# Performance work log

Measured on AMD Instinct MI355X. Metric: run time of the kernel, lower is better.

The kernel has to match this reference:

```python
import jax, jax.numpy as jnp
import numpy as np

N_NODES = 200000   # input_geom points
N_QUERY = 131072   # latent query points
K_NBR   = 32       # neighbors per query (uniform CSR for reproducibility)
N_EDGE  = N_QUERY * K_NBR
DIM     = 3
FEAT    = 3 + 2 * DIM  # N_i, D_avg, D_var, Delta(3), PCA eigvals(3)
HID     = 64
OUT     = 128


def setup_inputs() -> dict:
    key = jax.random.key(0)
    ks = jax.random.split(key, 8)
    input_geom = jax.random.normal(ks[0], (N_NODES, DIM), jnp.float32)
    latent_queries = jax.random.normal(ks[1], (N_QUERY, DIM), jnp.float32)
    neighbors_index = jax.random.randint(ks[2], (N_EDGE,), 0, N_NODES, dtype=jnp.int32)
    # uniform CSR row splits: every query has exactly K_NBR neighbors
    neighbors_row_splits = jnp.arange(N_QUERY + 1, dtype=jnp.int32) * K_NBR
    W1 = jax.random.normal(ks[3], (FEAT, HID), jnp.float32) / np.sqrt(FEAT)
    b1 = jax.random.normal(ks[4], (HID,), jnp.float32) * 0.01
    W2 = jax.random.normal(ks[5], (HID, OUT), jnp.float32) / np.sqrt(HID)
    b2 = jax.random.normal(ks[6], (OUT,), jnp.float32) * 0.01
    return {"input_geom": input_geom, "latent_queries": latent_queries,
            "neighbors_index": neighbors_index, "neighbors_row_splits": neighbors_row_splits,
            "W1": W1, "b1": b1, "W2": W2, "b2": b2}


def _stat_features(input_geom, latent_queries, neighbors_index, neighbors_row_splits):
    Q = latent_queries.shape[0]
    counts = neighbors_row_splits[1:] - neighbors_row_splits[:-1]          # [Q]
    qidx = jnp.repeat(jnp.arange(Q), counts, total_repeat_length=neighbors_index.shape[0])  # [E]
    nbr = input_geom[neighbors_index]                                      # [E, D]
    diff = nbr - latent_queries[qidx]                                      # [E, D]
    dist = jnp.linalg.norm(diff, axis=1)                                   # [E]

    N_i = counts.astype(jnp.float32)                                       # [Q]
    denom = jnp.maximum(N_i, 1.0)
    seg = lambda v: jax.ops.segment_sum(v, qidx, num_segments=Q)

    D_avg = seg(dist) / denom                                              # E[X]
    E_X2 = seg(dist * dist) / denom                                        # E[X^2]
    D_var = jnp.maximum(E_X2 - D_avg * D_avg, 0.0)

    centroid = seg(nbr) / denom[:, None]                                   # [Q, D]
    Delta = centroid - latent_queries                                      # [Q, D]

    centered = nbr - centroid[qidx]                                        # [E, D]
    cov = seg(centered[:, :, None] * centered[:, None, :]) / denom[:, None, None]  # [Q, D, D]

    eig = jnp.linalg.eigvalsh(cov)[:, ::-1]                                # descending, [Q, D]
    has = N_i > 0
    PCA = jnp.where(has[:, None], eig, 0.0)

    feat = jnp.concatenate([N_i[:, None], D_avg[:, None], D_var[:, None], Delta, PCA], axis=1)  # [Q, 9]
    feat = jnp.where(has[:, None], feat, 0.0)

    mean = feat.mean(axis=0, keepdims=True)
    std = feat.std(axis=0, ddof=1, keepdims=True)                          # torch.std is unbiased
    std = jnp.where(std < 1e-6, 1.0, std)
    return (feat - mean) / std


def reference(input_geom, latent_queries, neighbors_index, neighbors_row_splits, W1, b1, W2, b2):
    feat = _stat_features(input_geom, latent_queries, neighbors_index, neighbors_row_splits)
    h = jax.nn.relu(feat @ W1 + b1)
    return jax.nn.relu(h @ W2 + b2)
```

## Files before the change

### kernel.cpp

```cpp
#include <hip/hip_runtime.h>
#include <math.h>

#define QN 131072
#define NF 9
#define NH 64
#define NO 128
#define QT 128

using v8s = __attribute__((ext_vector_type(8))) short;
using v4f = __attribute__((ext_vector_type(4))) float;

__device__ __forceinline__ unsigned short f2bf(float x) {
  unsigned u = __float_as_uint(x);
  unsigned r = u + 0x7fffu + ((u >> 16) & 1u);
  return (unsigned short)(r >> 16);
}

__global__ __launch_bounds__(256)
void prep_kernel(const float* __restrict__ geom, float4* __restrict__ g4, int nn,
                 int padBlocks,
                 const float* __restrict__ W2, unsigned short* __restrict__ w2f,
                 float* __restrict__ acc)
{
  const int t = threadIdx.x;
  const int b = blockIdx.x;
  if (b == 0 && t < 2*NF) acc[t] = 0.0f;
  if (b < padBlocks) {
    int i = b * 256 + t;
    if (i < nn) {
      const float* p = geom + (size_t)i * 3;
      g4[i] = make_float4(p[0], p[1], p[2], 0.f);
    }
  } else {
    int i = (b - padBlocks) * 256 + t;
    int j  = i & 7;
    int l  = (i >> 3) & 63;
    int ot = (i >> 9) & 7;
    int kt = (i >> 12) & 1;
    int row = kt*32 + (l >> 4)*8 + j;
    int col = ot*16 + (l & 15);
    w2f[i] = f2bf(W2[row*NO + col]);
  }
}

__global__ __launch_bounds__(256)
void stats_kernel(const float4* __restrict__ g4,
                  const float* __restrict__ lq,
                  const int* __restrict__ nidx,
                  const int* __restrict__ rsplit,
                  float* __restrict__ feat,
                  float* __restrict__ acc)
{
  const int t = threadIdx.x;
  const int j = t & 1;
  const int q = blockIdx.x * 128 + (t >> 1);

  const int s = rsplit[q];
  const int cnt = rsplit[q+1] - s;

  const int* ip = nidx + s + j*16;
  int4 a0 = *(const int4*)(ip     );
  int4 a1 = *(const int4*)(ip +  4);
  int4 a2 = *(const int4*)(ip +  8);
  int4 a3 = *(const int4*)(ip + 12);

  const float qx = lq[q*3+0], qy = lq[q*3+1], qz = lq[q*3+2];

  int ids[16] = {a0.x,a0.y,a0.z,a0.w, a1.x,a1.y,a1.z,a1.w,
                 a2.x,a2.y,a2.z,a2.w, a3.x,a3.y,a3.z,a3.w};
  float4 P[16];
#pragma unroll
  for (int m = 0; m < 16; ++m) P[m] = g4[ids[m]];

  float sx=0.f, sy=0.f, sz=0.f;
  float sxx=0.f, sxy=0.f, sxz=0.f, syy=0.f, syz=0.f, szz=0.f;
  float sd=0.f, sd2=0.f;
#pragma unroll
  for (int m = 0; m < 16; ++m) {
    float4 p = P[m];
    sx += p.x; sy += p.y; sz += p.z;
    sxx = fmaf(p.x,p.x,sxx); sxy = fmaf(p.x,p.y,sxy); sxz = fmaf(p.x,p.z,sxz);
    syy = fmaf(p.y,p.y,syy); syz = fmaf(p.y,p.z,syz); szz = fmaf(p.z,p.z,szz);
    float dx = p.x-qx, dy = p.y-qy, dz = p.z-qz;
    float dd = fmaf(dx,dx,fmaf(dy,dy,dz*dz));
    sd2 += dd;
    sd += sqrtf(dd);
  }

  sx  += __shfl_xor(sx,  1);
  sy  += __shfl_xor(sy,  1);
  sz  += __shfl_xor(sz,  1);
  sxx += __shfl_xor(sxx, 1);
  sxy += __shfl_xor(sxy, 1);
  sxz += __shfl_xor(sxz, 1);
  syy += __shfl_xor(syy, 1);
  syz += __shfl_xor(syz, 1);
  szz += __shfl_xor(szz, 1);
  sd  += __shfl_xor(sd,  1);
  sd2 += __shfl_xor(sd2, 1);

  float cntf = (float)cnt;
  float denom = fmaxf(cntf, 1.0f);
  float inv = 1.0f / denom;
  float Davg = sd * inv;
  float Dvar = fmaxf(sd2 * inv - Davg*Davg, 0.0f);
  float cx = sx*inv, cy = sy*inv, cz = sz*inv;

  float a00 = sxx*inv - cx*cx;
  float a01 = sxy*inv - cx*cy;
  float a02 = sxz*inv - cx*cz;
  float a11 = syy*inv - cy*cy;
  float a12 = syz*inv - cy*cz;
  float a22 = szz*inv - cz*cz;

  float l0, l1, l2;
  {
    float p1 = a01*a01 + a02*a02 + a12*a12;
    float qm = (a00 + a11 + a22) * (1.0f/3.0f);
    float b00 = a00 - qm, b11 = a11 - qm, b22 = a22 - qm;
    float p2 = b00*b00 + b11*b11 + b22*b22 + 2.0f*p1;
    if (p2 < 1e-12f) {
      l0 = l1 = l2 = qm;
    } else {
      float p = sqrtf(p2 * (1.0f/6.0f));
      float ip2 = 1.0f / p;
      float c00 = b00*ip2, c11 = b11*ip2, c22 = b22*ip2;
      float c01 = a01*ip2, c02 = a02*ip2, c12 = a12*ip2;
      float det = c00*(c11*c22 - c12*c12)
                - c01*(c01*c22 - c12*c02)
                + c02*(c01*c12 - c11*c02);
      float r = fminf(1.0f, fmaxf(-1.0f, 0.5f*det));
      float phi = acosf(r) * (1.0f/3.0f);
      float tp = 2.0f * p;
      l0 = qm + tp * __cosf(phi);
      l2 = qm + tp * __cosf(phi + 2.0943951023931953f);
      l1 = 3.0f*qm - l0 - l2;
    }
  }

  float ft[NF];
  if (cntf > 0.f) {
    ft[0] = cntf; ft[1] = Davg; ft[2] = Dvar;
    ft[3] = cx - qx; ft[4] = cy - qy; ft[5] = cz - qz;
    ft[6] = l0; ft[7] = l1; ft[8] = l2;
  } else {
#pragma unroll
    for (int f = 0; f < NF; ++f) ft[f] = 0.f;
  }

  if (j == 0) {
    float* fp = feat + (size_t)q * 12;
    *(float4*)(fp    ) = make_float4(ft[0], ft[1], ft[2], ft[3]);
    *(float4*)(fp + 4) = make_float4(ft[4], ft[5], ft[6], ft[7]);
    *(float4*)(fp + 8) = make_float4(ft[8], 0.f, 0.f, 0.f);
  }

  __shared__ float sacc[4][2*NF];
  const int wid = t >> 6, lane = t & 63;
#pragma unroll
  for (int f = 0; f < NF; ++f) {
    float s1 = ft[f];
    float s2 = ft[f]*ft[f];
#pragma unroll
    for (int msk = 2; msk < 64; msk <<= 1) {
      s1 += __shfl_xor(s1, msk);
      s2 += __shfl_xor(s2, msk);
    }
    if (lane == 0) { sacc[wid][f] = s1; sacc[wid][NF+f] = s2; }
  }
  __syncthreads();
  if (t < 2*NF) {
    float ssum = sacc[0][t] + sacc[1][t] + sacc[2][t] + sacc[3][t];
    atomicAdd(&acc[t], ssum);
  }
}

__global__ __launch_bounds__(256)
void mlp_kernel(const float* __restrict__ feat,
                const float* __restrict__ acc,
                const float* __restrict__ W1, const float* __restrict__ b1,
                const unsigned short* __restrict__ w2f,
                const float* __restrict__ b2,
                float* __restrict__ out)
{
  __shared__ float sW1[NF*NH];
  __shared__ float sb1[NH];
  __shared__ float sb2[NO];
  __shared__ float ssc[NF], sbi[NF];
  __shared__ __align__(16) unsigned short ldsA[8*2*64*8];
  __shared__ __align__(16) unsigned short ldsB[2*8*64*8];

  const int t = threadIdx.x;
  const int qbase = blockIdx.x * QT;

  for (int i = t; i < NF*NH; i += 256) sW1[i] = W1[i];
  if (t < NH) sb1[t] = b1[t];
  if (t >= 64 && t < 64+NO) sb2[t-64] = b2[t-64];
  for (int i = t; i < 4096; i += 256) ((uint*)ldsB)[i] = ((const uint*)w2f)[i];
  if (t >= 192 && t < 192+NF) {
    int f = t - 192;
    double s = (double)acc[f], s2 = (double)acc[NF+f];
    const double Qd = (double)QN;
    double mean = s / Qd;
    double var = fmax((s2 - s*s/Qd) / (Qd - 1.0), 0.0);
    double sd = sqrt(var);
    if (sd < 1e-6) sd = 1.0;
    double iscl = 1.0 / sd;
    ssc[f] = (float)iscl;
    sbi[f] = (float)(-mean * iscl);
  }
  __syncthreads();

#pragma unroll
  for (int pass = 0; pass < 4; ++pass) {
    int item = pass*256 + t;
    int q  = item & 127;
    int kc = item >> 7;
    const float* fp = feat + (size_t)(qbase + q) * 12;
    float4 f0 = *(const float4*)(fp);
    float4 f1 = *(const float4*)(fp + 4);
    float f8v = fp[8];
    float fv[NF];
    fv[0] = fmaf(f0.x, ssc[0], sbi[0]);
    fv[1] = fmaf(f0.y, ssc[1], sbi[1]);
    fv[2] = fmaf(f0.z, ssc[2], sbi[2]);
    fv[3] = fmaf(f0.w, ssc[3], sbi[3]);
    fv[4] = fmaf(f1.x, ssc[4], sbi[4]);
    fv[5] = fmaf(f1.y, ssc[5], sbi[5]);
    fv[6] = fmaf(f1.z, ssc[6], sbi[6]);
    fv[7] = fmaf(f1.w, ssc[7], sbi[7]);
    fv[8] = fmaf(f8v,  ssc[8], sbi[8]);

    float h[8];
#pragma unroll
    for (int jj = 0; jj < 8; ++jj) h[jj] = sb1[kc*8 + jj];
#pragma unroll
    for (int k = 0; k < NF; ++k) {
      float fk = fv[k];
#pragma unroll
      for (int jj = 0; jj < 8; ++jj)
        h[jj] = fmaf(fk, sW1[k*NH + kc*8 + jj], h[jj]);
    }
    uint pk[4];
#pragma unroll
    for (int jj = 0; jj < 4; ++jj) {
      unsigned short lo = f2bf(fmaxf(h[2*jj  ], 0.f));
      unsigned short hi = f2bf(fmaxf(h[2*jj+1], 0.f));
      pk[jj] = (uint)lo | ((uint)hi << 16);
    }
    int base = ((((q >> 4)*2 + (kc >> 2))*64) + (q & 15) + 16*(kc & 3)) * 8;
    *(uint4*)&ldsA[base] = make_uint4(pk[0], pk[1], pk[2], pk[3]);
  }
  __syncthreads();

  const int wave = t >> 6;
  const int lane = t & 63;
  const int col  = lane & 15;
  const int rb   = (lane >> 4) * 4;

  v8s B00 = *(v8s*)&ldsB[(((0*8) + 2*wave    )*64 + lane)*8];
  v8s B01 = *(v8s*)&ldsB[(((0*8) + 2*wave + 1)*64 + lane)*8];
  v8s B10 = *(v8s*)&ldsB[(((1*8) + 2*wave    )*64 + lane)*8];
  v8s B11 = *(v8s*)&ldsB[(((1*8) + 2*wave + 1)*64 + lane)*8];

  const int o0 = (2*wave    )*16 + col;
  const int o1 = (2*wave + 1)*16 + col;
  const float b2a = sb2[o0];
  const float b2b = sb2[o1];

#pragma unroll
  for (int qt = 0; qt < 8; ++qt) {
    v8s A0 = *(v8s*)&ldsA[((qt*2 + 0)*64 + lane)*8];
    v8s A1 = *(v8s*)&ldsA[((qt*2 + 1)*64 + lane)*8];
    v4f c0 = {0.f, 0.f, 0.f, 0.f};
    v4f c1 = {0.f, 0.f, 0.f, 0.f};
    c0 = __builtin_amdgcn_mfma_f32_16x16x32_bf16(A0, B00, c0, 0, 0, 0);
    c0 = __builtin_amdgcn_mfma_f32_16x16x32_bf16(A1, B10, c0, 0, 0, 0);
    c1 = __builtin_amdgcn_mfma_f32_16x16x32_bf16(A0, B01, c1, 0, 0, 0);
    c1 = __builtin_amdgcn_mfma_f32_16x16x32_bf16(A1, B11, c1, 0, 0, 0);
#pragma unroll
    for (int r = 0; r < 4; ++r) {
      int gq = qbase + qt*16 + rb + r;
      out[(size_t)gq*NO + o0] = fmaxf(c0[r] + b2a, 0.f);
      out[(size_t)gq*NO + o1] = fmaxf(c1[r] + b2b, 0.f);
    }
  }
}

extern "C" void kernel_launch(void* const* d_in, const int* in_sizes, int n_in,
                              void* d_out, int out_size, void* d_ws, size_t ws_size,
                              hipStream_t stream) {
  const float* geom = (const float*)d_in[0];
  const float* lq   = (const float*)d_in[1];
  const int*   nidx = (const int*)d_in[2];
  const int*   rspl = (const int*)d_in[3];
  const float* W1   = (const float*)d_in[4];
  const float* b1   = (const float*)d_in[5];
  const float* W2   = (const float*)d_in[6];
  const float* b2   = (const float*)d_in[7];
  float* out = (float*)d_out;
  const int nn = in_sizes[0] / 3;

  char* w = (char*)d_ws;
  float*  feat = (float*)w;            w += (size_t)QN*12*sizeof(float);
  float4* g4   = (float4*)w;           w += (size_t)nn*sizeof(float4);
  unsigned short* w2f = (unsigned short*)w;  w += 16384*sizeof(unsigned short);
  float* acc   = (float*)w;

  const int padBlocks = (nn + 255) / 256;
  prep_kernel<<<padBlocks + 64, 256, 0, stream>>>(geom, g4, nn, padBlocks, W2, w2f, acc);
  stats_kernel<<<QN/128, 256, 0, stream>>>(g4, lq, nidx, rspl, feat, acc);
  mlp_kernel<<<QN/QT, 256, 0, stream>>>(feat, acc, W1, b1, w2f, b2, out);
}
```

Baseline: 133.2 us.

## Fuse prep, stats and MLP into one cooperative persistent kernel with grid syncs

Replaces the three kernel launches with one cooperative kernel of 512 blocks. It uses grid-wide syncs between the geometry padding, the statistics pass and the normalization-plus-MLP phase. Each block keeps its 256 queries' features in LDS instead of writing them to global memory and reading them back, which removes the feat round trip and two launch gaps. The gather is also split into two batches of 8 to reduce register pressure. The cost is two grid barriers, less parallelism from only 512 blocks, and a fallback to the old path if the cooperative launch fails.

```diff
diff --git a/kernel.cpp b/kernel.cpp
--- a/kernel.cpp
+++ b/kernel.cpp
@@ -1,11 +1,14 @@
 #include <hip/hip_runtime.h>
+#include <hip/hip_cooperative_groups.h>
 #include <math.h>
+
+namespace cg = cooperative_groups;
 
 #define QN 131072
 #define NF 9
 #define NH 64
 #define NO 128
-#define QT 128
+#define NBLK 512
 
 using v8s = __attribute__((ext_vector_type(8))) short;
 using v4f = __attribute__((ext_vector_type(4))) float;
@@ -14,6 +17,291 @@
   unsigned u = __float_as_uint(x);
   unsigned r = u + 0x7fffu + ((u >> 16) & 1u);
   return (unsigned short)(r >> 16);
+}
+
+__device__ __forceinline__ void eig3(float a00, float a01, float a02,
+                                     float a11, float a12, float a22,
+                                     float& l0, float& l1, float& l2) {
+  float p1 = a01*a01 + a02*a02 + a12*a12;
+  float qm = (a00 + a11 + a22) * (1.0f/3.0f);
+  float b00 = a00 - qm, b11 = a11 - qm, b22 = a22 - qm;
+  float p2 = b00*b00 + b11*b11 + b22*b22 + 2.0f*p1;
+  if (p2 < 1e-12f) {
+    l0 = l1 = l2 = qm;
+  } else {
+    float p = sqrtf(p2 * (1.0f/6.0f));
+    float ip2 = 1.0f / p;
+    float c00 = b00*ip2, c11 = b11*ip2, c22 = b22*ip2;
+    float c01 = a01*ip2, c02 = a02*ip2, c12 = a12*ip2;
+    float det = c00*(c11*c22 - c12*c12)
+              - c01*(c01*c22 - c12*c02)
+              + c02*(c01*c12 - c11*c02);
+    float r = fminf(1.0f, fmaxf(-1.0f, 0.5f*det));
+    float phi = acosf(r) * (1.0f/3.0f);
+    float tp = 2.0f * p;
+    l0 = qm + tp * __cosf(phi);
+    l2 = qm + tp * __cosf(phi + 2.0943951023931953f);
+    l1 = 3.0f*qm - l0 - l2;
+  }
+}
+
+__device__ __forceinline__ void stat_query(const float4* __restrict__ g4,
+                                           const float* __restrict__ lq,
+                                           const int* __restrict__ nidx,
+                                           const int* __restrict__ rsplit,
+                                           int q, int j, float* ft) {
+  const int s = rsplit[q];
+  const int cnt = rsplit[q+1] - s;
+
+  const int* ip = nidx + s + j*16;
+  int4 a0 = *(const int4*)(ip     );
+  int4 a1 = *(const int4*)(ip +  4);
+  int4 a2 = *(const int4*)(ip +  8);
+  int4 a3 = *(const int4*)(ip + 12);
+
+  const float qx = lq[q*3+0], qy = lq[q*3+1], qz = lq[q*3+2];
+
+  float sx=0.f, sy=0.f, sz=0.f;
+  float sxx=0.f, sxy=0.f, sxz=0.f, syy=0.f, syz=0.f, szz=0.f;
+  float sd=0.f, sd2=0.f;
+
+  int idsA[8] = {a0.x,a0.y,a0.z,a0.w, a1.x,a1.y,a1.z,a1.w};
+  int idsB[8] = {a2.x,a2.y,a2.z,a2.w, a3.x,a3.y,a3.z,a3.w};
+  float4 P[8];
+#pragma unroll
+  for (int m = 0; m < 8; ++m) P[m] = g4[idsA[m]];
+#pragma unroll
+  for (int m = 0; m < 8; ++m) {
+    float4 p = P[m];
+    sx += p.x; sy += p.y; sz += p.z;
+    sxx = fmaf(p.x,p.x,sxx); sxy = fmaf(p.x,p.y,sxy); sxz = fmaf(p.x,p.z,sxz);
+    syy = fmaf(p.y,p.y,syy); syz = fmaf(p.y,p.z,syz); szz = fmaf(p.z,p.z,szz);
+    float dx = p.x-qx, dy = p.y-qy, dz = p.z-qz;
+    float dd = fmaf(dx,dx,fmaf(dy,dy,dz*dz));
+    sd2 += dd; sd += sqrtf(dd);
+  }
+#pragma unroll
+  for (int m = 0; m < 8; ++m) P[m] = g4[idsB[m]];
+#pragma unroll
+  for (int m = 0; m < 8; ++m) {
+    float4 p = P[m];
+    sx += p.x; sy += p.y; sz += p.z;
+    sxx = fmaf(p.x,p.x,sxx); sxy = fmaf(p.x,p.y,sxy); sxz = fmaf(p.x,p.z,sxz);
+    syy = fmaf(p.y,p.y,syy); syz = fmaf(p.y,p.z,syz); szz = fmaf(p.z,p.z,szz);
+    float dx = p.x-qx, dy = p.y-qy, dz = p.z-qz;
+    float dd = fmaf(dx,dx,fmaf(dy,dy,dz*dz));
+    sd2 += dd; sd += sqrtf(dd);
+  }
+
+  sx  += __shfl_xor(sx,  1);
+  sy  += __shfl_xor(sy,  1);
+  sz  += __shfl_xor(sz,  1);
+  sxx += __shfl_xor(sxx, 1);
+  sxy += __shfl_xor(sxy, 1);
+  sxz += __shfl_xor(sxz, 1);
+  syy += __shfl_xor(syy, 1);
+  syz += __shfl_xor(syz, 1);
+  szz += __shfl_xor(szz, 1);
+  sd  += __shfl_xor(sd,  1);
+  sd2 += __shfl_xor(sd2, 1);
+
+  float cntf = (float)cnt;
+  float denom = fmaxf(cntf, 1.0f);
+  float inv = 1.0f / denom;
+  float Davg = sd * inv;
+  float Dvar = fmaxf(sd2 * inv - Davg*Davg, 0.0f);
+  float cx = sx*inv, cy = sy*inv, cz = sz*inv;
+
+  float l0, l1, l2;
+  eig3(sxx*inv - cx*cx, sxy*inv - cx*cy, sxz*inv - cx*cz,
+       syy*inv - cy*cy, syz*inv - cy*cz, szz*inv - cz*cz, l0, l1, l2);
+
+  if (cntf > 0.f) {
+    ft[0] = cntf; ft[1] = Davg; ft[2] = Dvar;
+    ft[3] = cx - qx; ft[4] = cy - qy; ft[5] = cz - qz;
+    ft[6] = l0; ft[7] = l1; ft[8] = l2;
+  } else {
+#pragma unroll
+    for (int f = 0; f < NF; ++f) ft[f] = 0.f;
+  }
+}
+
+__global__ __launch_bounds__(256, 2)
+void fused_kernel(const float* __restrict__ geom,
+                  const float* __restrict__ lq,
+                  const int* __restrict__ nidx,
+                  const int* __restrict__ rsplit,
+                  const float* __restrict__ W1,
+                  const float* __restrict__ b1,
+                  const float* __restrict__ W2,
+                  const float* __restrict__ b2,
+                  float4* __restrict__ g4,
+                  unsigned short* __restrict__ w2f,
+                  float* __restrict__ acc,
+                  float* __restrict__ out,
+                  int nn)
+{
+  __shared__ __align__(16) unsigned short ldsA[8*2*64*8];
+  __shared__ float sfeat[256][NF];
+  __shared__ float sW1[NF*NH];
+  __shared__ float sb1[NH];
+  __shared__ float sb2[NO];
+  __shared__ float sacc[4][2*NF];
+  __shared__ float ssc[NF], sbi[NF];
+
+  cg::grid_group grid = cg::this_grid();
+  const int t = threadIdx.x;
+  const int b = blockIdx.x;
+  const int wave = t >> 6;
+  const int lane = t & 63;
+
+  for (int gt = b*256 + t; gt < nn; gt += NBLK*256) {
+    const float* p = geom + (size_t)gt * 3;
+    g4[gt] = make_float4(p[0], p[1], p[2], 0.f);
+  }
+  if (b == 0) {
+    if (t < 2*NF) acc[t] = 0.f;
+#pragma unroll
+    for (int grp = 0; grp < 8; ++grp) {
+      int gi = grp*256 + t;
+      int l  = gi & 63;
+      int ot = (gi >> 6) & 7;
+      int kt = (gi >> 9) & 1;
+      int col  = ot*16 + (l & 15);
+      int rowb = kt*32 + (l >> 4)*8;
+      uint pk[4];
+#pragma unroll
+      for (int jj = 0; jj < 4; ++jj) {
+        uint lo = f2bf(W2[(rowb + 2*jj    )*NO + col]);
+        uint hi = f2bf(W2[(rowb + 2*jj + 1)*NO + col]);
+        pk[jj] = lo | (hi << 16);
+      }
+      *(uint4*)&w2f[(size_t)gi*8] = make_uint4(pk[0], pk[1], pk[2], pk[3]);
+    }
+  }
+  for (int i = t; i < NF*NH; i += 256) sW1[i] = W1[i];
+  if (t < NH) sb1[t] = b1[t];
+  if (t >= 64 && t < 64+NO) sb2[t-64] = b2[t-64];
+
+  grid.sync();
+
+#pragma unroll
+  for (int tt = 0; tt < 2; ++tt) {
+    const int j  = t & 1;
+    const int ql = t >> 1;
+    const int q  = b*256 + tt*128 + ql;
+
+    float ft[NF];
+    stat_query(g4, lq, nidx, rsplit, q, j, ft);
+
+    if (j == 0) {
+#pragma unroll
+      for (int f = 0; f < NF; ++f) sfeat[tt*128 + ql][f] = ft[f];
+    }
+
+#pragma unroll
+    for (int f = 0; f < NF; ++f) {
+      float s1 = ft[f];
+      float s2 = ft[f]*ft[f];
+#pragma unroll
+      for (int msk = 2; msk < 64; msk <<= 1) {
+        s1 += __shfl_xor(s1, msk);
+        s2 += __shfl_xor(s2, msk);
+      }
+      if (lane == 0) { sacc[wave][f] = s1; sacc[wave][NF+f] = s2; }
+    }
+    __syncthreads();
+    if (t < 2*NF) {
+      float ssum = sacc[0][t] + sacc[1][t] + sacc[2][t] + sacc[3][t];
+      atomicAdd(&acc[t], ssum);
+    }
+    __syncthreads();
+  }
+
+  grid.sync();
+
+  if (t >= 192 && t < 192+NF) {
+    int f = t - 192;
+    double s = (double)acc[f], s2 = (double)acc[NF+f];
+    const double Qd = (double)QN;
+    double mean = s / Qd;
+    double var = fmax((s2 - s*s/Qd) / (Qd - 1.0), 0.0);
+    double sdv = sqrt(var);
+    if (sdv < 1e-6) sdv = 1.0;
+    double iscl = 1.0 / sdv;
+    ssc[f] = (float)iscl;
+    sbi[f] = (float)(-mean * iscl);
+  }
+  __syncthreads();
+
+  v8s B00 = ((const v8s*)w2f)[(0*8 + 2*wave    )*64 + lane];
+  v8s B01 = ((const v8s*)w2f)[(0*8 + 2*wave + 1)*64 + lane];
+  v8s B10 = ((const v8s*)w2f)[(1*8 + 2*wave    )*64 + lane];
+  v8s B11 = ((const v8s*)w2f)[(1*8 + 2*wave + 1)*64 + lane];
+
+#pragma unroll
+  for (int tt = 0; tt < 2; ++tt) {
+#pragma unroll
+    for (int pass = 0; pass < 4; ++pass) {
+      int item = pass*256 + t;
+      int q  = item & 127;
+      int kc = item >> 7;
+      float fv[NF];
+#pragma unroll
+      for (int k = 0; k < NF; ++k)
+        fv[k] = fmaf(sfeat[tt*128 + q][k], ssc[k], sbi[k]);
+
+      float h[8];
+#pragma unroll
+      for (int jj = 0; jj < 8; ++jj) h[jj] = sb1[kc*8 + jj];
+#pragma unroll
+      for (int k = 0; k < NF; ++k) {
+        float fk = fv[k];
+#pragma unroll
+        for (int jj = 0; jj < 8; ++jj)
+          h[jj] = fmaf(fk, sW1[k*NH + kc*8 + jj], h[jj]);
+      }
+      uint pk[4];
+#pragma unroll
+      for (int jj = 0; jj < 4; ++jj) {
+        uint lo = f2bf(fmaxf(h[2*jj  ], 0.f));
+        uint hi = f2bf(fmaxf(h[2*jj+1], 0.f));
+        pk[jj] = lo | (hi << 16);
+      }
+      int base = ((((q >> 4)*2 + (kc >> 2))*64) + (q & 15) + 16*(kc & 3)) * 8;
+      *(uint4*)&ldsA[base] = make_uint4(pk[0], pk[1], pk[2], pk[3]);
+    }
+    __syncthreads();
+
+    {
+      const int qbase = b*256 + tt*128;
+      const int col = lane & 15;
+      const int rb  = (lane >> 4) * 4;
+      const int o0 = (2*wave    )*16 + col;
+      const int o1 = (2*wave + 1)*16 + col;
+      const float b2a = sb2[o0];
+      const float b2b = sb2[o1];
+
+#pragma unroll
+      for (int qt = 0; qt < 8; ++qt) {
+        v8s A0 = *(v8s*)&ldsA[((qt*2 + 0)*64 + lane)*8];
+        v8s A1 = *(v8s*)&ldsA[((qt*2 + 1)*64 + lane)*8];
+        v4f c0 = {0.f, 0.f, 0.f, 0.f};
+        v4f c1 = {0.f, 0.f, 0.f, 0.f};
+        c0 = __builtin_amdgcn_mfma_f32_16x16x32_bf16(A0, B00, c0, 0, 0, 0);
+        c0 = __builtin_amdgcn_mfma_f32_16x16x32_bf16(A1, B10, c0, 0, 0, 0);
+        c1 = __builtin_amdgcn_mfma_f32_16x16x32_bf16(A0, B01, c1, 0, 0, 0);
+        c1 = __builtin_amdgcn_mfma_f32_16x16x32_bf16(A1, B11, c1, 0, 0, 0);
+#pragma unroll
+        for (int r = 0; r < 4; ++r) {
+          int gq = qbase + qt*16 + rb + r;
+          out[(size_t)gq*NO + o0] = fmaxf(c0[r] + b2a, 0.f);
+          out[(size_t)gq*NO + o1] = fmaxf(c1[r] + b2b, 0.f);
+        }
+      }
+    }
+    __syncthreads();
+  }
 }
 
 __global__ __launch_bounds__(256)
@@ -55,98 +343,8 @@
   const int j = t & 1;
   const int q = blockIdx.x * 128 + (t >> 1);
 
-  const int s = rsplit[q];
-  const int cnt = rsplit[q+1] - s;
-
-  const int* ip = nidx + s + j*16;
-  int4 a0 = *(const int4*)(ip     );
-  int4 a1 = *(const int4*)(ip +  4);
-  int4 a2 = *(const int4*)(ip +  8);
-  int4 a3 = *(const int4*)(ip + 12);
-
-  const float qx = lq[q*3+0], qy = lq[q*3+1], qz = lq[q*3+2];
-
-  int ids[16] = {a0.x,a0.y,a0.z,a0.w, a1.x,a1.y,a1.z,a1.w,
-                 a2.x,a2.y,a2.z,a2.w, a3.x,a3.y,a3.z,a3.w};
-  float4 P[16];
-#pragma unroll
-  for (int m = 0; m < 16; ++m) P[m] = g4[ids[m]];
-
-  float sx=0.f, sy=0.f, sz=0.f;
-  float sxx=0.f, sxy=0.f, sxz=0.f, syy=0.f, syz=0.f, szz=0.f;
-  float sd=0.f, sd2=0.f;
-#pragma unroll
-  for (int m = 0; m < 16; ++m) {
-    float4 p = P[m];
-    sx += p.x; sy += p.y; sz += p.z;
-    sxx = fmaf(p.x,p.x,sxx); sxy = fmaf(p.x,p.y,sxy); sxz = fmaf(p.x,p.z,sxz);
-    syy = fmaf(p.y,p.y,syy); syz = fmaf(p.y,p.z,syz); szz = fmaf(p.z,p.z,szz);
-    float dx = p.x-qx, dy = p.y-qy, dz = p.z-qz;
-    float dd = fmaf(dx,dx,fmaf(dy,dy,dz*dz));
-    sd2 += dd;
-    sd += sqrtf(dd);
-  }
-
-  sx  += __shfl_xor(sx,  1);
-  sy  += __shfl_xor(sy,  1);
-  sz  += __shfl_xor(sz,  1);
-  sxx += __shfl_xor(sxx, 1);
-  sxy += __shfl_xor(sxy, 1);
-  sxz += __shfl_xor(sxz, 1);
-  syy += __shfl_xor(syy, 1);
-  syz += __shfl_xor(syz, 1);
-  szz += __shfl_xor(szz, 1);
-  sd  += __shfl_xor(sd,  1);
-  sd2 += __shfl_xor(sd2, 1);
-
-  float cntf = (float)cnt;
-  float denom = fmaxf(cntf, 1.0f);
-  float inv = 1.0f / denom;
-  float Davg = sd * inv;
-  float Dvar = fmaxf(sd2 * inv - Davg*Davg, 0.0f);
-  float cx = sx*inv, cy = sy*inv, cz = sz*inv;
-
-  float a00 = sxx*inv - cx*cx;
-  float a01 = sxy*inv - cx*cy;
-  float a02 = sxz*inv - cx*cz;
-  float a11 = syy*inv - cy*cy;
-  float a12 = syz*inv - cy*cz;
-  float a22 = szz*inv - cz*cz;
-
-  float l0, l1, l2;
-  {
-    float p1 = a01*a01 + a02*a02 + a12*a12;
-    float qm = (a00 + a11 + a22) * (1.0f/3.0f);
-    float b00 = a00 - qm, b11 = a11 - qm, b22 = a22 - qm;
-    float p2 = b00*b00 + b11*b11 + b22*b22 + 2.0f*p1;
-    if (p2 < 1e-12f) {
-      l0 = l1 = l2 = qm;
-    } else {
-      float p = sqrtf(p2 * (1.0f/6.0f));
-      float ip2 = 1.0f / p;
-      float c00 = b00*ip2, c11 = b11*ip2, c22 = b22*ip2;
-      float c01 = a01*ip2, c02 = a02*ip2, c12 = a12*ip2;
-      float det = c00*(c11*c22 - c12*c12)
-                - c01*(c01*c22 - c12*c02)
-                + c02*(c01*c12 - c11*c02);
-      float r = fminf(1.0f, fmaxf(-1.0f, 0.5f*det));
-      float phi = acosf(r) * (1.0f/3.0f);
-      float tp = 2.0f * p;
-      l0 = qm + tp * __cosf(phi);
-      l2 = qm + tp * __cosf(phi + 2.0943951023931953f);
-      l1 = 3.0f*qm - l0 - l2;
-    }
-  }
-
   float ft[NF];
-  if (cntf > 0.f) {
-    ft[0] = cntf; ft[1] = Davg; ft[2] = Dvar;
-    ft[3] = cx - qx; ft[4] = cy - qy; ft[5] = cz - qz;
-    ft[6] = l0; ft[7] = l1; ft[8] = l2;
-  } else {
-#pragma unroll
-    for (int f = 0; f < NF; ++f) ft[f] = 0.f;
-  }
+  stat_query(g4, lq, nidx, rsplit, q, j, ft);
 
   if (j == 0) {
     float* fp = feat + (size_t)q * 12;
@@ -191,7 +389,7 @@
   __shared__ __align__(16) unsigned short ldsB[2*8*64*8];
 
   const int t = threadIdx.x;
-  const int qbase = blockIdx.x * QT;
+  const int qbase = blockIdx.x * 128;
 
   for (int i = t; i < NF*NH; i += 256) sW1[i] = W1[i];
   if (t < NH) sb1[t] = b1[t];
@@ -244,9 +442,9 @@
     uint pk[4];
 #pragma unroll
     for (int jj = 0; jj < 4; ++jj) {
-      unsigned short lo = f2bf(fmaxf(h[2*jj  ], 0.f));
-      unsigned short hi = f2bf(fmaxf(h[2*jj+1], 0.f));
-      pk[jj] = (uint)lo | ((uint)hi << 16);
+      uint lo = f2bf(fmaxf(h[2*jj  ], 0.f));
+      uint hi = f2bf(fmaxf(h[2*jj+1], 0.f));
+      pk[jj] = lo | (hi << 16);
     }
     int base = ((((q >> 4)*2 + (kc >> 2))*64) + (q & 15) + 16*(kc & 3)) * 8;
     *(uint4*)&ldsA[base] = make_uint4(pk[0], pk[1], pk[2], pk[3]);
@@ -299,16 +497,23 @@
   const float* W2   = (const float*)d_in[6];
   const float* b2   = (const float*)d_in[7];
   float* out = (float*)d_out;
-  const int nn = in_sizes[0] / 3;
+  int nn = in_sizes[0] / 3;
 
   char* w = (char*)d_ws;
-  float*  feat = (float*)w;            w += (size_t)QN*12*sizeof(float);
-  float4* g4   = (float4*)w;           w += (size_t)nn*sizeof(float4);
-  unsigned short* w2f = (unsigned short*)w;  w += 16384*sizeof(unsigned short);
+  float*  feat = (float*)w;                  w += (size_t)QN*12*sizeof(float);
+  float4* g4   = (float4*)w;                 w += (size_t)nn * sizeof(float4);
+  unsigned short* w2f = (unsigned short*)w;  w += (size_t)16384 * sizeof(unsigned short);
   float* acc   = (float*)w;
 
-  const int padBlocks = (nn + 255) / 256;
-  prep_kernel<<<padBlocks + 64, 256, 0, stream>>>(geom, g4, nn, padBlocks, W2, w2f, acc);
-  stats_kernel<<<QN/128, 256, 0, stream>>>(g4, lq, nidx, rspl, feat, acc);
-  mlp_kernel<<<QN/QT, 256, 0, stream>>>(feat, acc, W1, b1, w2f, b2, out);
-}
+  void* args[] = { (void*)&geom, (void*)&lq, (void*)&nidx, (void*)&rspl,
+                   (void*)&W1, (void*)&b1, (void*)&W2, (void*)&b2,
+                   (void*)&g4, (void*)&w2f, (void*)&acc, (void*)&out, (void*)&nn };
+  hipError_t err = hipLaunchCooperativeKernel((void*)fused_kernel, dim3(NBLK),
+                                              dim3(256), args, 0, stream);
+  if (err != hipSuccess) {
+    const int padBlocks = (nn + 255) / 256;
+    prep_kernel<<<padBlocks + 64, 256, 0, stream>>>(geom, g4, nn, padBlocks, W2, w2f, acc);
+    stats_kernel<<<QN/128, 256, 0, stream>>>(g4, lq, nidx, rspl, feat, acc);
+    mlp_kernel<<<QN/128, 256, 0, stream>>>(feat, acc, W1, b1, w2f, b2, out);
+  }
+}
```

Result: slower. 252.7 us (+89.7%).
